# Optimization experiments

Hardware: AMD Instinct MI355X
Metric: run time of the kernel (lower is better)

The kernel has to match this reference:

```python
import jax, jax.numpy as jnp
import numpy as np

N, D_IN, D_H = 8192, 512, 512


def setup_inputs() -> dict:
    key = jax.random.key(0)
    kH, kWq, kbq, kWk, kbk = jax.random.split(key, 5)
    s_in = 1.0 / np.sqrt(D_IN)
    return {
        "H": jax.random.normal(kH, (N, D_IN), dtype=jnp.float32),
        "Wq": jax.random.normal(kWq, (D_IN, D_H), dtype=jnp.float32) * s_in,
        "bq": jax.random.normal(kbq, (D_H,), dtype=jnp.float32) * 0.01,
        "Wk": jax.random.normal(kWk, (D_IN, D_H), dtype=jnp.float32) * s_in,
        "bk": jax.random.normal(kbk, (D_H,), dtype=jnp.float32) * 0.01,
    }


def reference(H, Wq, bq, Wk, bk):
    # H: [N, T]; Q, K: [N, d_h]
    Q = H @ Wq + bq
    K = H @ Wk + bk
    # A: [N, N] raw scores
    A = Q @ K.T
    n = A.shape[0]
    # torch.where(eye, 0, A): zero out the diagonal BEFORE scale/softmax
    A = A.at[jnp.arange(n), jnp.arange(n)].set(0.0)
    A = A / jnp.sqrt(jnp.asarray(K.shape[-1], A.dtype))
    A = jax.nn.softmax(A, axis=-1)
    # aggregate values (= H itself) and add residual
    return A @ H + H
```

## Files before the change

### kernel.cpp

```cpp
#include <hip/hip_runtime.h>
#include <cstdint>
#include <cstddef>

#define GLOBAL_AS __attribute__((address_space(1)))
#define LDS_AS __attribute__((address_space(3)))

typedef __attribute__((ext_vector_type(8))) short short8;
typedef __attribute__((ext_vector_type(4))) float floatx4;
typedef __attribute__((ext_vector_type(2))) long long2v;
typedef __attribute__((ext_vector_type(4))) int int4v;
typedef __attribute__((ext_vector_type(8))) int int8v;

#if defined(__has_builtin)
#if __has_builtin(__builtin_amdgcn_cvt_pk_fp8_f32)
#define HAVE_HW_FP8 1
#endif
#endif

static __device__ __forceinline__ unsigned short f2bf(float f) {
  uint32_t u = __builtin_bit_cast(uint32_t, f);
  u += 0x7fffu + ((u >> 16) & 1u);
  return (unsigned short)(u >> 16);
}

static __device__ __forceinline__ unsigned char f2fp8(float f) {
#ifdef HAVE_HW_FP8
  float c = fminf(fmaxf(f, -448.f), 448.f);
  return (unsigned char)(__builtin_amdgcn_cvt_pk_fp8_f32(c, 0.f, 0, false) & 0xff);
#else
  unsigned char s = 0;
  if (f < 0.f) { s = 0x80; f = -f; }
  if (f >= 448.f) return s | 0x7e;
  if (f < 0.015625f) { int r = (int)(f * 512.f + 0.5f); return s | (unsigned char)r; }
  uint32_t u = __builtin_bit_cast(uint32_t, f);
  int e = (int)((u >> 23) & 0xff) - 127;
  uint32_t keep = (u >> 20) & 7, rest = u & 0xfffffu;
  if (rest > 0x80000u || (rest == 0x80000u && (keep & 1))) ++keep;
  if (keep == 8) { keep = 0; ++e; }
  if (e > 8) return s | 0x7e;
  return s | (unsigned char)(((e + 7) << 3) | keep);
#endif
}

static __device__ __forceinline__ uint32_t pack4fp8(const float e[4]) {
#ifdef HAVE_HW_FP8
  const uint32_t p01 = (uint32_t)__builtin_amdgcn_cvt_pk_fp8_f32(e[0], e[1], 0, false);
  const uint32_t p23 = (uint32_t)__builtin_amdgcn_cvt_pk_fp8_f32(e[2], e[3], 0, false);
  return (p01 & 0xffffu) | (p23 << 16);
#else
  return (uint32_t)f2fp8(e[0]) | ((uint32_t)f2fp8(e[1]) << 8) |
         ((uint32_t)f2fp8(e[2]) << 16) | ((uint32_t)f2fp8(e[3]) << 24);
#endif
}


static __device__ __forceinline__ void wait_vm0() {
  __builtin_amdgcn_s_waitcnt(0x0f70);
}

static __device__ __forceinline__ int8v load_frag32(const unsigned char* base, int row, int quad) {
  const int h = row & 7;
  const int c0 = (2 * quad) ^ h;
  const int c1 = (2 * quad + 1) ^ h;
  const int4v lo = *(const int4v*)(base + row * 128 + c0 * 16);
  const int4v hi = *(const int4v*)(base + row * 128 + c1 * 16);
  int8v r;
  r[0] = lo[0]; r[1] = lo[1]; r[2] = lo[2]; r[3] = lo[3];
  r[4] = hi[0]; r[5] = hi[1]; r[6] = hi[2]; r[7] = hi[3];
  return r;
}

static __device__ __forceinline__ floatx4 mx_mfma(int8v a, int8v b, floatx4 c) {
  return __builtin_amdgcn_mfma_scale_f32_16x16x128_f8f6f4(a, b, c, 0, 0, 0, 0x7f, 0, 0x7f);
}

__global__ __launch_bounds__(256) void transpose_h_kernel(
    const float* __restrict__ in, unsigned char* __restrict__ outT8,
    unsigned short* __restrict__ outN, int R, int C) {
  __shared__ float t[64][65];
  const int bc = blockIdx.x * 64;
  const int br = blockIdx.y * 64;
  const int tc = threadIdx.x & 63;
  const int tr = threadIdx.x >> 6;
  for (int r = tr; r < 64; r += 4) {
    const float v = in[(size_t)(br + r) * C + bc + tc];
    t[r][tc] = v;
    outN[(size_t)(br + r) * C + bc + tc] = f2bf(v);
  }
  __syncthreads();
  const int tperm = 4 * (tc & 15) + (tc >> 4);
  for (int r = tr; r < 64; r += 4)
    outT8[(size_t)(bc + r) * R + br + tperm] = f2fp8(t[tc][r]);
}

__global__ __launch_bounds__(256) void transpose_w_kernel(
    const float* __restrict__ in, unsigned short* __restrict__ outT, int R, int C) {
  __shared__ float t[64][65];
  const int bc = blockIdx.x * 64;
  const int br = blockIdx.y * 64;
  const int tc = threadIdx.x & 63;
  const int tr = threadIdx.x >> 6;
  for (int r = tr; r < 64; r += 4)
    t[r][tc] = in[(size_t)(br + r) * C + bc + tc];
  __syncthreads();
  for (int r = tr; r < 64; r += 4)
    outT[(size_t)(bc + r) * R + br + tc] = f2bf(t[tc][r]);
}

__global__ __launch_bounds__(256) void pack_bias_kernel(
    const float* __restrict__ bq, const float* __restrict__ bk,
    float* __restrict__ bqk) {
  int i = blockIdx.x * 256 + threadIdx.x;
  bqk[i] = (i < 512) ? bq[i] : bk[i - 512];
}

__global__ __launch_bounds__(256, 4) void gemm_proj(
    const unsigned short* __restrict__ A,
    const unsigned short* __restrict__ Bt,
    int Ncols, int K,
    const float* __restrict__ bias,
    unsigned char* __restrict__ C8)
{
  __shared__ unsigned short As[2][128 * 32];
  __shared__ unsigned short Bs[2][128 * 32];

  const int tid  = threadIdx.x;
  const int lane = tid & 63;
  const int wave = tid >> 6;
  const int wr   = (wave >> 1) * 64;
  const int wc   = (wave & 1) * 64;
  const int quad = lane >> 4;
  const int l15  = lane & 15;
  const int bm   = blockIdx.y * 128;
  const int bn   = blockIdx.x * 128;

  const int c0 = tid, c1 = tid + 256;
  const int r0a = c0 >> 2, k0a = (((c0 & 3) ^ ((c0 >> 3) & 3)) << 3);
  const int r1a = c1 >> 2, k1a = (((c1 & 3) ^ ((c1 >> 3) & 3)) << 3);

  auto stage = [&](int kt, int b) {
    __builtin_amdgcn_global_load_lds(
        (const GLOBAL_AS void*)(A + (size_t)(bm + r0a) * K + kt + k0a),
        (LDS_AS void*)(&As[b][c0 * 8]), 16, 0, 0);
    __builtin_amdgcn_global_load_lds(
        (const GLOBAL_AS void*)(A + (size_t)(bm + r1a) * K + kt + k1a),
        (LDS_AS void*)(&As[b][c1 * 8]), 16, 0, 0);
    __builtin_amdgcn_global_load_lds(
        (const GLOBAL_AS void*)(Bt + (size_t)(bn + r0a) * K + kt + k0a),
        (LDS_AS void*)(&Bs[b][c0 * 8]), 16, 0, 0);
    __builtin_amdgcn_global_load_lds(
        (const GLOBAL_AS void*)(Bt + (size_t)(bn + r1a) * K + kt + k1a),
        (LDS_AS void*)(&Bs[b][c1 * 8]), 16, 0, 0);
  };

  floatx4 acc[4][4];
#pragma unroll
  for (int i = 0; i < 4; ++i)
#pragma unroll
    for (int j = 0; j < 4; ++j)
      acc[i][j] = (floatx4){0.f, 0.f, 0.f, 0.f};

  stage(0, 0);
  const int swq = quad ^ ((l15 >> 1) & 3);
  const int nIter = K >> 5;
  for (int it = 0; it < nIter; ++it) {
    const int b = it & 1;
    wait_vm0();
    __syncthreads();
    if (it + 1 < nIter) stage((it + 1) << 5, b ^ 1);

    short8 af[4], bfr[4];
#pragma unroll
    for (int i = 0; i < 4; ++i)
      af[i] = *(const short8*)(&As[b][(wr + i * 16 + l15) * 32 + swq * 8]);
#pragma unroll
    for (int j = 0; j < 4; ++j)
      bfr[j] = *(const short8*)(&Bs[b][(wc + j * 16 + l15) * 32 + swq * 8]);
#pragma unroll
    for (int i = 0; i < 4; ++i)
#pragma unroll
      for (int j = 0; j < 4; ++j)
        acc[i][j] = __builtin_amdgcn_mfma_f32_16x16x32_bf16(af[i], bfr[j], acc[i][j], 0, 0, 0);
  }

#pragma unroll
  for (int i = 0; i < 4; ++i) {
    const int rl = bm + wr + i * 16 + quad * 4;
#pragma unroll
    for (int r = 0; r < 4; ++r) {
      const int row = rl + r;
      float e[4];
#pragma unroll
      for (int j = 0; j < 4; ++j)
        e[j] = acc[i][j][r] + bias[bn + wc + j * 16 + l15];
      const uint32_t d = pack4fp8(e);
      *(uint32_t*)(C8 + (size_t)row * Ncols + bn + wc + 4 * l15) = d;
    }
  }
}

__global__ __launch_bounds__(256, 4) void gemm_qk8(
    const unsigned char* __restrict__ A,
    const unsigned char* __restrict__ Bt,
    int Ncols, int K, int lda, int ldb,
    float* __restrict__ lsum,
    int row0,
    unsigned char* __restrict__ P8)
{
  __shared__ unsigned char As[2][128 * 64];
  __shared__ unsigned char Bs[2][128 * 64];

  const int tid  = threadIdx.x;
  const int lane = tid & 63;
  const int wave = tid >> 6;
  const int wr   = (wave >> 1) * 64;
  const int wc   = (wave & 1) * 64;
  const int quad = lane >> 4;
  const int l15  = lane & 15;

  int bxn = blockIdx.x, byn = blockIdx.y;
  if (gridDim.x == 64 && gridDim.y == 64) {
    const int id = blockIdx.y * 64 + blockIdx.x;
    const int r = id & 7, w = id >> 3;
    bxn = (r & 3) * 16 + (w & 15);
    byn = (r >> 2) * 32 + (w >> 4);
  }
  const int bm = byn * 128;
  const int bn = bxn * 128;

  const int c0 = tid, c1 = tid + 256;
  const int r0a = c0 >> 2, k0a = (((c0 & 3) ^ ((c0 >> 3) & 3)) << 4);
  const int r1a = c1 >> 2, k1a = (((c1 & 3) ^ ((c1 >> 3) & 3)) << 4);

  auto stage = [&](int kt, int b) {
    __builtin_amdgcn_global_load_lds(
        (const GLOBAL_AS void*)(A + (size_t)(bm + r0a) * lda + kt + k0a),
        (LDS_AS void*)(&As[b][c0 * 16]), 16, 0, 0);
    __builtin_amdgcn_global_load_lds(
        (const GLOBAL_AS void*)(A + (size_t)(bm + r1a) * lda + kt + k1a),
        (LDS_AS void*)(&As[b][c1 * 16]), 16, 0, 0);
    __builtin_amdgcn_global_load_lds(
        (const GLOBAL_AS void*)(Bt + (size_t)(bn + r0a) * ldb + kt + k0a),
        (LDS_AS void*)(&Bs[b][c0 * 16]), 16, 0, 0);
    __builtin_amdgcn_global_load_lds(
        (const GLOBAL_AS void*)(Bt + (size_t)(bn + r1a) * ldb + kt + k1a),
        (LDS_AS void*)(&Bs[b][c1 * 16]), 16, 0, 0);
  };

  floatx4 acc[4][4];
#pragma unroll
  for (int i = 0; i < 4; ++i)
#pragma unroll
    for (int j = 0; j < 4; ++j)
      acc[i][j] = (floatx4){0.f, 0.f, 0.f, 0.f};

  stage(0, 0);
  const int swq = quad ^ ((l15 >> 1) & 3);
  const int nIter = K >> 6;
  for (int it = 0; it < nIter; ++it) {
    const int b = it & 1;
    wait_vm0();
    __syncthreads();
    if (it + 1 < nIter) stage((it + 1) << 6, b ^ 1);

    long2v af[4], bfr[4];
#pragma unroll
    for (int i = 0; i < 4; ++i)
      af[i] = *(const long2v*)(&As[b][(wr + i * 16 + l15) * 64 + swq * 16]);
#pragma unroll
    for (int j = 0; j < 4; ++j)
      bfr[j] = *(const long2v*)(&Bs[b][(wc + j * 16 + l15) * 64 + swq * 16]);
#pragma unroll
    for (int i = 0; i < 4; ++i)
#pragma unroll
      for (int j = 0; j < 4; ++j) {
        acc[i][j] = __builtin_amdgcn_mfma_f32_16x16x32_fp8_fp8(af[i].x, bfr[j].x, acc[i][j], 0, 0, 0);
        acc[i][j] = __builtin_amdgcn_mfma_f32_16x16x32_fp8_fp8(af[i].y, bfr[j].y, acc[i][j], 0, 0, 0);
      }
  }

  const float scale = 0.044194173824159216f;
#pragma unroll
  for (int i = 0; i < 4; ++i) {
    const int rl = bm + wr + i * 16 + quad * 4;
#pragma unroll
    for (int r = 0; r < 4; ++r) {
      const int row = rl + r;
      float e4[4];
#pragma unroll
      for (int j = 0; j < 4; ++j) {
        const int col = bn + wc + j * 16 + l15;
        const float lg = ((row0 + row) == col) ? 0.f : acc[i][j][r] * scale;
        e4[j] = fminf(__expf(lg), 448.f);
      }
      float rsum = (e4[0] + e4[1]) + (e4[2] + e4[3]);
      const uint32_t d = pack4fp8(e4);
      *(uint32_t*)(P8 + (size_t)row * Ncols + bn + wc + 4 * l15) = d;
      rsum += __shfl_xor(rsum, 1);
      rsum += __shfl_xor(rsum, 2);
      rsum += __shfl_xor(rsum, 4);
      rsum += __shfl_xor(rsum, 8);
      if (l15 == 0) atomicAdd(&lsum[row0 + row], rsum);
    }
  }
}

template <bool DIRECT>
__global__ __launch_bounds__(256, 3) void gemm_pv8(
    const unsigned char* __restrict__ P,
    const unsigned char* __restrict__ Bt,
    int Kchunk,
    const float* __restrict__ lvec,
    const float* __restrict__ Hres,
    int row0,
    float* __restrict__ outp,
    size_t partStride)
{
  __shared__ unsigned char As[2][64 * 128];
  __shared__ unsigned char Bs[2][128 * 128];

  const int tid  = threadIdx.x;
  const int lane = tid & 63;
  const int wave = tid >> 6;
  const int wr   = (wave >> 1) * 32;
  const int wc   = (wave & 1) * 64;
  const int quad = lane >> 4;
  const int l15  = lane & 15;

  int bxn = blockIdx.x, byn = blockIdx.y;
  if (gridDim.x == 4 && gridDim.y == 128) {
    const int id2 = blockIdx.y * 4 + blockIdx.x;
    const int xcd = id2 & 7, w = id2 >> 3;
    bxn = w & 3;
    byn = xcd * 16 + (w >> 2);
  }
  const int bm = byn * 64;
  const int bn = bxn * 128;
  const int k0 = blockIdx.z * Kchunk;

  float* part = outp + (DIRECT ? 0 : (size_t)blockIdx.z * partStride);

  const int a0 = tid, a1 = tid + 256;
  const int ar0 = a0 >> 3, ac0 = ((a0 & 7) ^ (ar0 & 7)) << 4;
  const int ar1 = a1 >> 3, ac1 = ((a1 & 7) ^ (ar1 & 7)) << 4;
  const int b0 = tid, b1 = tid + 256, b2 = tid + 512, b3 = tid + 768;
  const int br0 = b0 >> 3, bc0 = ((b0 & 7) ^ (br0 & 7)) << 4;
  const int br1 = b1 >> 3, bc1 = ((b1 & 7) ^ (br1 & 7)) << 4;
  const int br2 = b2 >> 3, bc2 = ((b2 & 7) ^ (br2 & 7)) << 4;
  const int br3 = b3 >> 3, bc3 = ((b3 & 7) ^ (br3 & 7)) << 4;

  auto stage = [&](int kt, int b) {
    __builtin_amdgcn_global_load_lds(
        (const GLOBAL_AS void*)(P + (size_t)(bm + ar0) * 8192 + kt + ac0),
        (LDS_AS void*)(&As[b][a0 * 16]), 16, 0, 0);
    __builtin_amdgcn_global_load_lds(
        (const GLOBAL_AS void*)(P + (size_t)(bm + ar1) * 8192 + kt + ac1),
        (LDS_AS void*)(&As[b][a1 * 16]), 16, 0, 0);
    __builtin_amdgcn_global_load_lds(
        (const GLOBAL_AS void*)(Bt + (size_t)(bn + br0) * 8192 + kt + bc0),
        (LDS_AS void*)(&Bs[b][b0 * 16]), 16, 0, 0);
    __builtin_amdgcn_global_load_lds(
        (const GLOBAL_AS void*)(Bt + (size_t)(bn + br1) * 8192 + kt + bc1),
        (LDS_AS void*)(&Bs[b][b1 * 16]), 16, 0, 0);
    __builtin_amdgcn_global_load_lds(
        (const GLOBAL_AS void*)(Bt + (size_t)(bn + br2) * 8192 + kt + bc2),
        (LDS_AS void*)(&Bs[b][b2 * 16]), 16, 0, 0);
    __builtin_amdgcn_global_load_lds(
        (const GLOBAL_AS void*)(Bt + (size_t)(bn + br3) * 8192 + kt + bc3),
        (LDS_AS void*)(&Bs[b][b3 * 16]), 16, 0, 0);
  };

  floatx4 acc[2][4];
#pragma unroll
  for (int i = 0; i < 2; ++i)
#pragma unroll
    for (int j = 0; j < 4; ++j)
      acc[i][j] = (floatx4){0.f, 0.f, 0.f, 0.f};

  stage(k0, 0);
  const int nIter = Kchunk >> 7;
  for (int it = 0; it < nIter; ++it) {
    const int b = it & 1;
    wait_vm0();
    __syncthreads();
    if (it + 1 < nIter) stage(k0 + ((it + 1) << 7), b ^ 1);

    const int8v af0 = load_frag32(As[b], wr + l15, quad);
    const int8v af1 = load_frag32(As[b], wr + 16 + l15, quad);
#pragma unroll
    for (int j = 0; j < 4; ++j) {
      const int8v bf = load_frag32(Bs[b], wc + j * 16 + l15, quad);
      acc[0][j] = mx_mfma(af0, bf, acc[0][j]);
      acc[1][j] = mx_mfma(af1, bf, acc[1][j]);
    }
  }

#pragma unroll
  for (int i = 0; i < 2; ++i) {
    const int rl = bm + wr + i * 16 + quad * 4;
#pragma unroll
    for (int j = 0; j < 4; ++j) {
      const int col = bn + wc + j * 16 + l15;
#pragma unroll
      for (int r = 0; r < 4; ++r) {
        const int row = rl + r;
        const float v = acc[i][j][r];
        if (DIRECT) {
          const int grow = row0 + row;
          part[(size_t)grow * 512 + col] =
              v / lvec[grow] + Hres[(size_t)grow * 512 + col];
        } else {
          part[(size_t)row * 512 + col] = v;
        }
      }
    }
  }
}

__global__ __launch_bounds__(256) void combine_kernel(
    const float* __restrict__ parts, size_t partStride, int S,
    const float* __restrict__ lvec, const float* __restrict__ Hres,
    float* __restrict__ out, int n4) {
  int i = blockIdx.x * 256 + threadIdx.x;
  if (i >= n4) return;
  float4 a = ((const float4*)parts)[i];
  for (int s = 1; s < S; ++s) {
    const float4 b = ((const float4*)(parts + (size_t)s * partStride))[i];
    a.x += b.x; a.y += b.y; a.z += b.z; a.w += b.w;
  }
  const int row = i >> 7;
  const float inv = 1.f / lvec[row];
  const float4 h = ((const float4*)Hres)[i];
  float4 o;
  o.x = a.x * inv + h.x;
  o.y = a.y * inv + h.y;
  o.z = a.z * inv + h.z;
  o.w = a.w * inv + h.w;
  ((float4*)out)[i] = o;
}

extern "C" void kernel_launch(void* const* d_in, const int* in_sizes, int n_in,
                              void* d_out, int out_size, void* d_ws, size_t ws_size,
                              hipStream_t stream) {
  const float* H  = (const float*)d_in[0];
  const float* Wq = (const float*)d_in[1];
  const float* bq = (const float*)d_in[2];
  const float* Wk = (const float*)d_in[3];
  const float* bk = (const float*)d_in[4];
  float* out = (float*)d_out;

  const int N = 8192, D = 512;

  char* ws = (char*)d_ws;
  size_t off = 0;
  auto alloc = [&](size_t bytes) { char* p = ws + off; off += bytes; return p; };
  unsigned short* Hb   = (unsigned short*)alloc((size_t)N * D * 2);
  unsigned char*  HbT8 = (unsigned char*)alloc((size_t)D * N);
  unsigned char*  QK8  = (unsigned char*)alloc((size_t)N * 2 * D);
  unsigned short* BqkT = (unsigned short*)alloc((size_t)2 * D * D * 2);
  float* bqk = (float*)alloc((size_t)2 * D * 4);
  float* l   = (float*)alloc((size_t)N * 4);
  const size_t base = off;
  unsigned char* P8 = (unsigned char*)(ws + base);

  const size_t pBytes = (size_t)N * N;
  const size_t partBytes = (size_t)N * D * 4;
  const size_t partStride = (size_t)N * D;
  const size_t avail = (ws_size > base) ? (ws_size - base) : 0;

  int S = 0;
  if (avail >= pBytes) {
    const size_t extra = avail - pBytes;
    S = (extra >= 2 * partBytes) ? 2 : 1;
  }
  float* parts = (float*)(ws + base + pBytes);

  hipMemsetAsync(l, 0, (size_t)N * 4, stream);
  transpose_h_kernel<<<dim3(D / 64, N / 64), 256, 0, stream>>>(H, HbT8, Hb, N, D);
  transpose_w_kernel<<<dim3(D / 64, D / 64), 256, 0, stream>>>(Wq, BqkT, D, D);
  transpose_w_kernel<<<dim3(D / 64, D / 64), 256, 0, stream>>>(Wk, BqkT + (size_t)D * D, D, D);
  pack_bias_kernel<<<dim3(4), 256, 0, stream>>>(bq, bk, bqk);

  gemm_proj<<<dim3(2 * D / 128, N / 128), 256, 0, stream>>>(
      Hb, BqkT, 2 * D, D, bqk, QK8);

  if (S >= 1) {
    gemm_qk8<<<dim3(N / 128, N / 128), 256, 0, stream>>>(
        QK8, QK8 + D, N, D, 2 * D, 2 * D, l, 0, P8);
    if (S == 1) {
      gemm_pv8<true><<<dim3(D / 128, N / 64, 1), 256, 0, stream>>>(
          P8, HbT8, N, l, H, 0, out, 0);
    } else {
      gemm_pv8<false><<<dim3(D / 128, N / 64, S), 256, 0, stream>>>(
          P8, HbT8, N / S, nullptr, nullptr, 0, parts, partStride);
      combine_kernel<<<dim3((N * D / 4 + 255) / 256), 256, 0, stream>>>(
          parts, partStride, S, l, H, out, N * D / 4);
    }
  } else {
    int maxRows = (int)(avail / (size_t)N);
    maxRows &= ~127;
    if (maxRows < 128) maxRows = 128;
    for (int r0 = 0; r0 < N; r0 += maxRows) {
      int rows = N - r0;
      if (rows > maxRows) rows = maxRows;
      gemm_qk8<<<dim3(N / 128, rows / 128), 256, 0, stream>>>(
          QK8 + (size_t)r0 * 2 * D, QK8 + D, N, D, 2 * D, 2 * D, l, r0, P8);
      gemm_pv8<true><<<dim3(D / 128, rows / 64, 1), 256, 0, stream>>>(
          P8, HbT8, N, l, H, r0, out, 0);
    }
  }
}
```

Baseline: 256.3 us.

## Replace split-K partial buffers and combine pass with atomic accumulation into output

The H transpose kernel now also writes H into the output buffer as the residual. The PV GEMM then atomically adds its normalized split-K partials (acc / l) directly into the output, which removes the partial buffers and the separate combine kernel. The two weight transposes are merged into one launch using blockIdx.z. This saves a full read and write pass over the partials plus two launches, at the cost of float atomics on every output element and order-dependent rounding.

```diff
diff --git a/kernel.cpp b/kernel.cpp
--- a/kernel.cpp
+++ b/kernel.cpp
@@ -76,7 +76,8 @@
 
 __global__ __launch_bounds__(256) void transpose_h_kernel(
     const float* __restrict__ in, unsigned char* __restrict__ outT8,
-    unsigned short* __restrict__ outN, int R, int C) {
+    unsigned short* __restrict__ outN, float* __restrict__ outF,
+    int R, int C) {
   __shared__ float t[64][65];
   const int bc = blockIdx.x * 64;
   const int br = blockIdx.y * 64;
@@ -86,6 +87,7 @@
     const float v = in[(size_t)(br + r) * C + bc + tc];
     t[r][tc] = v;
     outN[(size_t)(br + r) * C + bc + tc] = f2bf(v);
+    outF[(size_t)(br + r) * C + bc + tc] = v;
   }
   __syncthreads();
   const int tperm = 4 * (tc & 15) + (tc >> 4);
@@ -93,18 +95,21 @@
     outT8[(size_t)(bc + r) * R + br + tperm] = f2fp8(t[tc][r]);
 }
 
-__global__ __launch_bounds__(256) void transpose_w_kernel(
-    const float* __restrict__ in, unsigned short* __restrict__ outT, int R, int C) {
+__global__ __launch_bounds__(256) void transpose_w2_kernel(
+    const float* __restrict__ Wq, const float* __restrict__ Wk,
+    unsigned short* __restrict__ outT, int Dd) {
+  const float* in = blockIdx.z ? Wk : Wq;
+  unsigned short* out = outT + (size_t)blockIdx.z * Dd * Dd;
   __shared__ float t[64][65];
   const int bc = blockIdx.x * 64;
   const int br = blockIdx.y * 64;
   const int tc = threadIdx.x & 63;
   const int tr = threadIdx.x >> 6;
   for (int r = tr; r < 64; r += 4)
-    t[r][tc] = in[(size_t)(br + r) * C + bc + tc];
+    t[r][tc] = in[(size_t)(br + r) * Dd + bc + tc];
   __syncthreads();
   for (int r = tr; r < 64; r += 4)
-    outT[(size_t)(bc + r) * R + br + tc] = f2bf(t[tc][r]);
+    out[(size_t)(bc + r) * Dd + br + tc] = f2bf(t[tc][r]);
 }
 
 __global__ __launch_bounds__(256) void pack_bias_kernel(
@@ -305,16 +310,13 @@
   }
 }
 
-template <bool DIRECT>
 __global__ __launch_bounds__(256, 3) void gemm_pv8(
     const unsigned char* __restrict__ P,
     const unsigned char* __restrict__ Bt,
     int Kchunk,
     const float* __restrict__ lvec,
-    const float* __restrict__ Hres,
     int row0,
-    float* __restrict__ outp,
-    size_t partStride)
+    float* __restrict__ out)
 {
   __shared__ unsigned char As[2][64 * 128];
   __shared__ unsigned char Bs[2][128 * 128];
@@ -337,8 +339,6 @@
   const int bm = byn * 64;
   const int bn = bxn * 128;
   const int k0 = blockIdx.z * Kchunk;
-
-  float* part = outp + (DIRECT ? 0 : (size_t)blockIdx.z * partStride);
 
   const int a0 = tid, a1 = tid + 256;
   const int ar0 = a0 >> 3, ac0 = ((a0 & 7) ^ (ar0 & 7)) << 4;
@@ -399,44 +399,16 @@
   for (int i = 0; i < 2; ++i) {
     const int rl = bm + wr + i * 16 + quad * 4;
 #pragma unroll
-    for (int j = 0; j < 4; ++j) {
-      const int col = bn + wc + j * 16 + l15;
-#pragma unroll
-      for (int r = 0; r < 4; ++r) {
-        const int row = rl + r;
-        const float v = acc[i][j][r];
-        if (DIRECT) {
-          const int grow = row0 + row;
-          part[(size_t)grow * 512 + col] =
-              v / lvec[grow] + Hres[(size_t)grow * 512 + col];
-        } else {
-          part[(size_t)row * 512 + col] = v;
-        }
+    for (int r = 0; r < 4; ++r) {
+      const int grow = row0 + rl + r;
+      const float inv = 1.f / lvec[grow];
+#pragma unroll
+      for (int j = 0; j < 4; ++j) {
+        const int col = bn + wc + j * 16 + l15;
+        atomicAdd(&out[(size_t)grow * 512 + col], acc[i][j][r] * inv);
       }
     }
   }
-}
-
-__global__ __launch_bounds__(256) void combine_kernel(
-    const float* __restrict__ parts, size_t partStride, int S,
-    const float* __restrict__ lvec, const float* __restrict__ Hres,
-    float* __restrict__ out, int n4) {
-  int i = blockIdx.x * 256 + threadIdx.x;
-  if (i >= n4) return;
-  float4 a = ((const float4*)parts)[i];
-  for (int s = 1; s < S; ++s) {
-    const float4 b = ((const float4*)(parts + (size_t)s * partStride))[i];
-    a.x += b.x; a.y += b.y; a.z += b.z; a.w += b.w;
-  }
-  const int row = i >> 7;
-  const float inv = 1.f / lvec[row];
-  const float4 h = ((const float4*)Hres)[i];
-  float4 o;
-  o.x = a.x * inv + h.x;
-  o.y = a.y * inv + h.y;
-  o.z = a.z * inv + h.z;
-  o.w = a.w * inv + h.w;
-  ((float4*)out)[i] = o;
 }
 
 extern "C" void kernel_launch(void* const* d_in, const int* in_sizes, int n_in,
@@ -464,38 +436,22 @@
   unsigned char* P8 = (unsigned char*)(ws + base);
 
   const size_t pBytes = (size_t)N * N;
-  const size_t partBytes = (size_t)N * D * 4;
-  const size_t partStride = (size_t)N * D;
   const size_t avail = (ws_size > base) ? (ws_size - base) : 0;
-
-  int S = 0;
-  if (avail >= pBytes) {
-    const size_t extra = avail - pBytes;
-    S = (extra >= 2 * partBytes) ? 2 : 1;
-  }
-  float* parts = (float*)(ws + base + pBytes);
+  const bool fullP = (avail >= pBytes);
 
   hipMemsetAsync(l, 0, (size_t)N * 4, stream);
-  transpose_h_kernel<<<dim3(D / 64, N / 64), 256, 0, stream>>>(H, HbT8, Hb, N, D);
-  transpose_w_kernel<<<dim3(D / 64, D / 64), 256, 0, stream>>>(Wq, BqkT, D, D);
-  transpose_w_kernel<<<dim3(D / 64, D / 64), 256, 0, stream>>>(Wk, BqkT + (size_t)D * D, D, D);
+  transpose_h_kernel<<<dim3(D / 64, N / 64), 256, 0, stream>>>(H, HbT8, Hb, out, N, D);
+  transpose_w2_kernel<<<dim3(D / 64, D / 64, 2), 256, 0, stream>>>(Wq, Wk, BqkT, D);
   pack_bias_kernel<<<dim3(4), 256, 0, stream>>>(bq, bk, bqk);
 
   gemm_proj<<<dim3(2 * D / 128, N / 128), 256, 0, stream>>>(
       Hb, BqkT, 2 * D, D, bqk, QK8);
 
-  if (S >= 1) {
+  if (fullP) {
     gemm_qk8<<<dim3(N / 128, N / 128), 256, 0, stream>>>(
         QK8, QK8 + D, N, D, 2 * D, 2 * D, l, 0, P8);
-    if (S == 1) {
-      gemm_pv8<true><<<dim3(D / 128, N / 64, 1), 256, 0, stream>>>(
-          P8, HbT8, N, l, H, 0, out, 0);
-    } else {
-      gemm_pv8<false><<<dim3(D / 128, N / 64, S), 256, 0, stream>>>(
-          P8, HbT8, N / S, nullptr, nullptr, 0, parts, partStride);
-      combine_kernel<<<dim3((N * D / 4 + 255) / 256), 256, 0, stream>>>(
-          parts, partStride, S, l, H, out, N * D / 4);
-    }
+    gemm_pv8<<<dim3(D / 128, N / 64, 2), 256, 0, stream>>>(
+        P8, HbT8, N / 2, l, 0, out);
   } else {
     int maxRows = (int)(avail / (size_t)N);
     maxRows &= ~127;
@@ -505,8 +461,8 @@
       if (rows > maxRows) rows = maxRows;
       gemm_qk8<<<dim3(N / 128, rows / 128), 256, 0, stream>>>(
           QK8 + (size_t)r0 * 2 * D, QK8 + D, N, D, 2 * D, 2 * D, l, r0, P8);
-      gemm_pv8<true><<<dim3(D / 128, rows / 64, 1), 256, 0, stream>>>(
-          P8, HbT8, N, l, H, r0, out, 0);
+      gemm_pv8<<<dim3(D / 128, rows / 64, 1), 256, 0, stream>>>(
+          P8, HbT8, N, l, r0, out);
     }
   }
 }
```

New measurement: 261.6 us. +2.1%, slower.

## Switch PV GEMM to fp8 16x16x32 MFMA with 64-wide K tiles

Applied to the files above, without the earlier changes.

Rewrites the P·H GEMM inner loop to use plain fp8 16x16x32 MFMAs instead of the block-scaled 16x16x128 f8f6f4 instruction. The K tile shrinks from 128 to 64 bytes with a new LDS swizzle, which cuts shared memory per block and raises the launch-bounds occupancy target from 3 to 4. It also merges the two weight-transpose launches into one grid with a z dimension. The trade is lower per-instruction MFMA throughput and twice as many K iterations and barriers, in exchange for more resident blocks and less LDS pressure.

```diff
diff --git a/kernel.cpp b/kernel.cpp
--- a/kernel.cpp
+++ b/kernel.cpp
@@ -8,8 +8,6 @@
 typedef __attribute__((ext_vector_type(8))) short short8;
 typedef __attribute__((ext_vector_type(4))) float floatx4;
 typedef __attribute__((ext_vector_type(2))) long long2v;
-typedef __attribute__((ext_vector_type(4))) int int4v;
-typedef __attribute__((ext_vector_type(8))) int int8v;
 
 #if defined(__has_builtin)
 #if __has_builtin(__builtin_amdgcn_cvt_pk_fp8_f32)
@@ -58,22 +56,6 @@
   __builtin_amdgcn_s_waitcnt(0x0f70);
 }
 
-static __device__ __forceinline__ int8v load_frag32(const unsigned char* base, int row, int quad) {
-  const int h = row & 7;
-  const int c0 = (2 * quad) ^ h;
-  const int c1 = (2 * quad + 1) ^ h;
-  const int4v lo = *(const int4v*)(base + row * 128 + c0 * 16);
-  const int4v hi = *(const int4v*)(base + row * 128 + c1 * 16);
-  int8v r;
-  r[0] = lo[0]; r[1] = lo[1]; r[2] = lo[2]; r[3] = lo[3];
-  r[4] = hi[0]; r[5] = hi[1]; r[6] = hi[2]; r[7] = hi[3];
-  return r;
-}
-
-static __device__ __forceinline__ floatx4 mx_mfma(int8v a, int8v b, floatx4 c) {
-  return __builtin_amdgcn_mfma_scale_f32_16x16x128_f8f6f4(a, b, c, 0, 0, 0, 0x7f, 0, 0x7f);
-}
-
 __global__ __launch_bounds__(256) void transpose_h_kernel(
     const float* __restrict__ in, unsigned char* __restrict__ outT8,
     unsigned short* __restrict__ outN, int R, int C) {
@@ -93,18 +75,21 @@
     outT8[(size_t)(bc + r) * R + br + tperm] = f2fp8(t[tc][r]);
 }
 
-__global__ __launch_bounds__(256) void transpose_w_kernel(
-    const float* __restrict__ in, unsigned short* __restrict__ outT, int R, int C) {
+__global__ __launch_bounds__(256) void transpose_w2_kernel(
+    const float* __restrict__ Wq, const float* __restrict__ Wk,
+    unsigned short* __restrict__ outT, int Dd) {
+  const float* in = blockIdx.z ? Wk : Wq;
+  unsigned short* out = outT + (size_t)blockIdx.z * Dd * Dd;
   __shared__ float t[64][65];
   const int bc = blockIdx.x * 64;
   const int br = blockIdx.y * 64;
   const int tc = threadIdx.x & 63;
   const int tr = threadIdx.x >> 6;
   for (int r = tr; r < 64; r += 4)
-    t[r][tc] = in[(size_t)(br + r) * C + bc + tc];
+    t[r][tc] = in[(size_t)(br + r) * Dd + bc + tc];
   __syncthreads();
   for (int r = tr; r < 64; r += 4)
-    outT[(size_t)(bc + r) * R + br + tc] = f2bf(t[tc][r]);
+    out[(size_t)(bc + r) * Dd + br + tc] = f2bf(t[tc][r]);
 }
 
 __global__ __launch_bounds__(256) void pack_bias_kernel(
@@ -306,7 +291,7 @@
 }
 
 template <bool DIRECT>
-__global__ __launch_bounds__(256, 3) void gemm_pv8(
+__global__ __launch_bounds__(256, 4) void gemm_pv8(
     const unsigned char* __restrict__ P,
     const unsigned char* __restrict__ Bt,
     int Kchunk,
@@ -316,8 +301,8 @@
     float* __restrict__ outp,
     size_t partStride)
 {
-  __shared__ unsigned char As[2][64 * 128];
-  __shared__ unsigned char Bs[2][128 * 128];
+  __shared__ unsigned char As[2][64 * 64];
+  __shared__ unsigned char Bs[2][128 * 64];
 
   const int tid  = threadIdx.x;
   const int lane = tid & 63;
@@ -340,34 +325,22 @@
 
   float* part = outp + (DIRECT ? 0 : (size_t)blockIdx.z * partStride);
 
-  const int a0 = tid, a1 = tid + 256;
-  const int ar0 = a0 >> 3, ac0 = ((a0 & 7) ^ (ar0 & 7)) << 4;
-  const int ar1 = a1 >> 3, ac1 = ((a1 & 7) ^ (ar1 & 7)) << 4;
-  const int b0 = tid, b1 = tid + 256, b2 = tid + 512, b3 = tid + 768;
-  const int br0 = b0 >> 3, bc0 = ((b0 & 7) ^ (br0 & 7)) << 4;
-  const int br1 = b1 >> 3, bc1 = ((b1 & 7) ^ (br1 & 7)) << 4;
-  const int br2 = b2 >> 3, bc2 = ((b2 & 7) ^ (br2 & 7)) << 4;
-  const int br3 = b3 >> 3, bc3 = ((b3 & 7) ^ (br3 & 7)) << 4;
+  const int ca = tid;
+  const int ar = ca >> 2, ak = (((ca & 3) ^ ((ca >> 3) & 3)) << 4);
+  const int cb0 = tid, cb1 = tid + 256;
+  const int br0 = cb0 >> 2, bk0 = (((cb0 & 3) ^ ((cb0 >> 3) & 3)) << 4);
+  const int br1 = cb1 >> 2, bk1 = (((cb1 & 3) ^ ((cb1 >> 3) & 3)) << 4);
 
   auto stage = [&](int kt, int b) {
     __builtin_amdgcn_global_load_lds(
-        (const GLOBAL_AS void*)(P + (size_t)(bm + ar0) * 8192 + kt + ac0),
-        (LDS_AS void*)(&As[b][a0 * 16]), 16, 0, 0);
-    __builtin_amdgcn_global_load_lds(
-        (const GLOBAL_AS void*)(P + (size_t)(bm + ar1) * 8192 + kt + ac1),
-        (LDS_AS void*)(&As[b][a1 * 16]), 16, 0, 0);
-    __builtin_amdgcn_global_load_lds(
-        (const GLOBAL_AS void*)(Bt + (size_t)(bn + br0) * 8192 + kt + bc0),
-        (LDS_AS void*)(&Bs[b][b0 * 16]), 16, 0, 0);
-    __builtin_amdgcn_global_load_lds(
-        (const GLOBAL_AS void*)(Bt + (size_t)(bn + br1) * 8192 + kt + bc1),
-        (LDS_AS void*)(&Bs[b][b1 * 16]), 16, 0, 0);
-    __builtin_amdgcn_global_load_lds(
-        (const GLOBAL_AS void*)(Bt + (size_t)(bn + br2) * 8192 + kt + bc2),
-        (LDS_AS void*)(&Bs[b][b2 * 16]), 16, 0, 0);
-    __builtin_amdgcn_global_load_lds(
-        (const GLOBAL_AS void*)(Bt + (size_t)(bn + br3) * 8192 + kt + bc3),
-        (LDS_AS void*)(&Bs[b][b3 * 16]), 16, 0, 0);
+        (const GLOBAL_AS void*)(P + (size_t)(bm + ar) * 8192 + kt + ak),
+        (LDS_AS void*)(&As[b][ca * 16]), 16, 0, 0);
+    __builtin_amdgcn_global_load_lds(
+        (const GLOBAL_AS void*)(Bt + (size_t)(bn + br0) * 8192 + kt + bk0),
+        (LDS_AS void*)(&Bs[b][cb0 * 16]), 16, 0, 0);
+    __builtin_amdgcn_global_load_lds(
+        (const GLOBAL_AS void*)(Bt + (size_t)(bn + br1) * 8192 + kt + bk1),
+        (LDS_AS void*)(&Bs[b][cb1 * 16]), 16, 0, 0);
   };
 
   floatx4 acc[2][4];
@@ -378,21 +351,28 @@
       acc[i][j] = (floatx4){0.f, 0.f, 0.f, 0.f};
 
   stage(k0, 0);
-  const int nIter = Kchunk >> 7;
+  const int swq = quad ^ ((l15 >> 1) & 3);
+  const int nIter = Kchunk >> 6;
   for (int it = 0; it < nIter; ++it) {
     const int b = it & 1;
     wait_vm0();
     __syncthreads();
-    if (it + 1 < nIter) stage(k0 + ((it + 1) << 7), b ^ 1);
-
-    const int8v af0 = load_frag32(As[b], wr + l15, quad);
-    const int8v af1 = load_frag32(As[b], wr + 16 + l15, quad);
-#pragma unroll
-    for (int j = 0; j < 4; ++j) {
-      const int8v bf = load_frag32(Bs[b], wc + j * 16 + l15, quad);
-      acc[0][j] = mx_mfma(af0, bf, acc[0][j]);
-      acc[1][j] = mx_mfma(af1, bf, acc[1][j]);
-    }
+    if (it + 1 < nIter) stage(k0 + ((it + 1) << 6), b ^ 1);
+
+    long2v af[2], bfr[4];
+#pragma unroll
+    for (int i = 0; i < 2; ++i)
+      af[i] = *(const long2v*)(&As[b][(wr + i * 16 + l15) * 64 + swq * 16]);
+#pragma unroll
+    for (int j = 0; j < 4; ++j)
+      bfr[j] = *(const long2v*)(&Bs[b][(wc + j * 16 + l15) * 64 + swq * 16]);
+#pragma unroll
+    for (int i = 0; i < 2; ++i)
+#pragma unroll
+      for (int j = 0; j < 4; ++j) {
+        acc[i][j] = __builtin_amdgcn_mfma_f32_16x16x32_fp8_fp8(af[i].x, bfr[j].x, acc[i][j], 0, 0, 0);
+        acc[i][j] = __builtin_amdgcn_mfma_f32_16x16x32_fp8_fp8(af[i].y, bfr[j].y, acc[i][j], 0, 0, 0);
+      }
   }
 
 #pragma unroll
@@ -477,8 +457,7 @@
 
   hipMemsetAsync(l, 0, (size_t)N * 4, stream);
   transpose_h_kernel<<<dim3(D / 64, N / 64), 256, 0, stream>>>(H, HbT8, Hb, N, D);
-  transpose_w_kernel<<<dim3(D / 64, D / 64), 256, 0, stream>>>(Wq, BqkT, D, D);
-  transpose_w_kernel<<<dim3(D / 64, D / 64), 256, 0, stream>>>(Wk, BqkT + (size_t)D * D, D, D);
+  transpose_w2_kernel<<<dim3(D / 64, D / 64, 2), 256, 0, stream>>>(Wq, Wk, BqkT, D);
   pack_bias_kernel<<<dim3(4), 256, 0, stream>>>(bq, bk, bqk);
 
   gemm_proj<<<dim3(2 * D / 128, N / 128), 256, 0, stream>>>(
```

After: 253.2 us (median of 2 runs). Within noise of the previous version (-1.2%).
